# Kernel optimization log

Hardware: AMD Instinct MI355X
Metric: run time of the kernel (lower is better)

Reference implementation:

```python
import jax, jax.numpy as jnp
import numpy as np

N, E, G = 20000, 320000, 50
IN, H1, D1, H2, D2 = 64, 10, 64, 1, 128
NEG_SLOPE = 0.2  # DGL GATConv default


def _edge_softmax(e, dst, n):
    # segment softmax of per-edge scores e[E,H] grouped by destination node
    m = jax.ops.segment_max(e, dst, num_segments=n)
    m = jnp.where(jnp.isfinite(m), m, 0.0)  # nodes with zero in-degree
    ex = jnp.exp(e - m[dst])
    s = jax.ops.segment_sum(ex, dst, num_segments=n)
    return ex / jnp.where(s > 0, s, 1.0)[dst]


def _gat_layer(feat, W, al, ar, b, src, dst, n, h, d):
    ft = (feat @ W).reshape(n, h, d)              # [N,H,D]
    el = (ft * al).sum(-1)                        # [N,H]
    er = (ft * ar).sum(-1)                        # [N,H]
    e = jax.nn.leaky_relu(el[src] + er[dst], NEG_SLOPE)  # [E,H]
    a = _edge_softmax(e, dst, n)                  # [E,H]
    out = jax.ops.segment_sum(ft[src] * a[:, :, None], dst, num_segments=n)
    return out + b.reshape(1, h, d)


def setup_inputs() -> dict:
    key = jax.random.key(0)
    ks = jax.random.split(key, 16)
    feat = jax.random.normal(ks[0], (N, IN), dtype=jnp.float32)
    src = jax.random.randint(ks[1], (E,), 0, N)
    dst = jax.random.randint(ks[2], (E,), 0, N)
    graph_ids = jnp.sort(jax.random.randint(ks[3], (N,), 0, G))
    s1 = 1.0 / np.sqrt(IN)
    W1 = jax.random.normal(ks[4], (IN, H1 * D1), dtype=jnp.float32) * s1
    al1 = jax.random.normal(ks[5], (H1, D1), dtype=jnp.float32) * 0.1
    ar1 = jax.random.normal(ks[6], (H1, D1), dtype=jnp.float32) * 0.1
    b1 = jnp.zeros((H1 * D1,), dtype=jnp.float32)
    W2 = jax.random.normal(ks[7], (D1, H2 * D2), dtype=jnp.float32) * (1.0 / np.sqrt(D1))
    al2 = jax.random.normal(ks[8], (H2, D2), dtype=jnp.float32) * 0.1
    ar2 = jax.random.normal(ks[9], (H2, D2), dtype=jnp.float32) * 0.1
    b2 = jnp.zeros((H2 * D2,), dtype=jnp.float32)
    lw1 = jax.random.normal(ks[10], (D2, D2), dtype=jnp.float32) * (1.0 / np.sqrt(D2))
    lb1 = jnp.zeros((D2,), dtype=jnp.float32)
    lw2 = jax.random.normal(ks[11], (D2, 1), dtype=jnp.float32) * (1.0 / np.sqrt(D2))
    lb2 = jnp.zeros((1,), dtype=jnp.float32)
    return {"feat": feat, "src": src, "dst": dst, "graph_ids": graph_ids,
            "W1": W1, "al1": al1, "ar1": ar1, "b1": b1,
            "W2": W2, "al2": al2, "ar2": ar2, "b2": b2,
            "lw1": lw1, "lb1": lb1, "lw2": lw2, "lb2": lb2}


def reference(feat, src, dst, graph_ids, W1, al1, ar1, b1, W2, al2, ar2, b2, lw1, lb1, lw2, lb2):
    # eval mode: all dropouts are identity
    h = _gat_layer(feat, W1, al1, ar1, b1, src, dst, N, H1, D1)  # [N,10,64]
    h = jax.nn.relu(h)
    h = h.sum(axis=1)                                            # [N,64]
    h = _gat_layer(h, W2, al2, ar2, b2, src, dst, N, H2, D2)     # [N,1,128]
    h = jax.nn.relu(h)
    # readout_nodes op='max' over each graph in the batch
    r = jax.ops.segment_max(h, graph_ids, num_segments=G)        # [G,1,128]
    r = jnp.where(jnp.isfinite(r), r, 0.0)
    r = jax.nn.relu(r @ lw1 + lb1)
    r = jax.nn.relu(r @ lw2 + lb2)                               # [G,1,1]
    return r.reshape(-1)
```

## Files before the change

### kernel.cpp

```cpp
#include <hip/hip_runtime.h>
#include <hip/hip_fp16.h>

#define NN 20000
#define EE 320000
#define GG 50
#define IN_ 64
#define H1_ 10
#define D1_ 64
#define D2_ 128
#define F1 640
#define NEG 0.2f
#define CAP 128

static inline int cdiv(long long a, int b){ return (int)((a + b - 1) / b); }

__device__ inline float lrelu(float x){ return x > 0.f ? x : NEG * x; }

__device__ inline void fma_mix_lo(float& acc, float packed, float a){
  asm("v_fma_mix_f32 %0, %1, %2, %0 op_sel_hi:[1,0,0]"
      : "+v"(acc) : "v"(packed), "v"(a));
}
__device__ inline void fma_mix_hi(float& acc, float packed, float a){
  asm("v_fma_mix_f32 %0, %1, %2, %0 op_sel:[1,0,0] op_sel_hi:[1,0,0]"
      : "+v"(acc) : "v"(packed), "v"(a));
}

__global__ __launch_bounds__(256) void fused1(
    const int* __restrict__ src, const int* __restrict__ dst,
    int* __restrict__ cur, int* __restrict__ ssrc,
    const float* __restrict__ feat, const float* __restrict__ W1,
    const float* __restrict__ al1, const float* __restrict__ ar1,
    __half* __restrict__ ft1h, float* __restrict__ elT, float* __restrict__ erT){
  __shared__ float AsT[64][68];
  __shared__ __half Bsh[64][68];
  int b = blockIdx.x;
  if(b < 1250){
    int e = b * 256 + threadIdx.x;
    int d = dst[e];
    int pos = atomicAdd(&cur[d], 1);
    if(pos < CAP) ssrc[(d << 7) + pos] = src[e];
    return;
  }
  int b2 = b - 1250;
  int h = b2 % H1_;
  int n0 = (b2 / H1_) * 64;
  int tid = threadIdx.x;
  #pragma unroll
  for(int l = 0; l < 4; l++){
    int idx = tid + l * 256;
    int r = idx >> 4, c4 = (idx & 15) << 2;
    float4 v = make_float4(0.f,0.f,0.f,0.f);
    if(n0 + r < NN) v = *(const float4*)&feat[(size_t)(n0 + r) * IN_ + c4];
    AsT[c4+0][r] = v.x; AsT[c4+1][r] = v.y; AsT[c4+2][r] = v.z; AsT[c4+3][r] = v.w;
    float4 w = *(const float4*)&W1[(size_t)(idx >> 4) * F1 + h * 64 + c4];
    union { __half2 h2[2]; float2 f2; } u;
    u.h2[0] = __floats2half2_rn(w.x, w.y);
    u.h2[1] = __floats2half2_rn(w.z, w.w);
    *(float2*)&Bsh[idx >> 4][c4] = u.f2;
  }
  __syncthreads();
  int tr = tid >> 4, tc = tid & 15;
  float acc[4][4];
  #pragma unroll
  for(int i = 0; i < 4; i++)
    #pragma unroll
    for(int j = 0; j < 4; j++) acc[i][j] = 0.f;
  #pragma unroll 8
  for(int k = 0; k < 64; k++){
    float4 a4 = *(const float4*)&AsT[k][tr << 2];
    float2 b2v = *(const float2*)&Bsh[k][tc << 2];
    float av[4] = {a4.x, a4.y, a4.z, a4.w};
    #pragma unroll
    for(int i = 0; i < 4; i++){
      fma_mix_lo(acc[i][0], b2v.x, av[i]);
      fma_mix_hi(acc[i][1], b2v.x, av[i]);
      fma_mix_lo(acc[i][2], b2v.y, av[i]);
      fma_mix_hi(acc[i][3], b2v.y, av[i]);
    }
  }
  float al4[4], ar4[4];
  #pragma unroll
  for(int j = 0; j < 4; j++){
    al4[j] = al1[h * 64 + (tc << 2) + j];
    ar4[j] = ar1[h * 64 + (tc << 2) + j];
  }
  #pragma unroll
  for(int i = 0; i < 4; i++){
    int row = n0 + (tr << 2) + i;
    bool ok = row < NN;
    if(ok){
      union { __half2 h2[2]; float2 f2; } u;
      u.h2[0] = __floats2half2_rn(acc[i][0], acc[i][1]);
      u.h2[1] = __floats2half2_rn(acc[i][2], acc[i][3]);
      *(float2*)&ft1h[((size_t)h * NN + row) * 64 + (tc << 2)] = u.f2;
    }
    float e1 = acc[i][0]*al4[0] + acc[i][1]*al4[1] + acc[i][2]*al4[2] + acc[i][3]*al4[3];
    float e2 = acc[i][0]*ar4[0] + acc[i][1]*ar4[1] + acc[i][2]*ar4[2] + acc[i][3]*ar4[3];
    #pragma unroll
    for(int off = 1; off < 16; off <<= 1){
      e1 += __shfl_xor(e1, off, 64);
      e2 += __shfl_xor(e2, off, 64);
    }
    if(tc == 0 && ok){
      elT[(size_t)h * NN + row] = e1;
      erT[(size_t)h * NN + row] = e2;
    }
  }
}

__global__ __launch_bounds__(256) void l1_head(
    const int* __restrict__ cur, const int* __restrict__ ssrc,
    const float* __restrict__ elT, const float* __restrict__ erT,
    const __half* __restrict__ ft1h, const float* __restrict__ b1,
    __half* __restrict__ out1h){
  __shared__ int2 pairs[4][2][2][32];
  int b = blockIdx.x;
  int xcd = b & 7, slot = b >> 3;
  int h, blk;
  if(slot < 1250){ h = xcd; blk = slot; }
  else {
    int s = slot - 1250; h = 8 + (xcd >> 2); blk = (xcd & 3) * 313 + s;
    if(blk >= 1250) return;
  }
  int wave = threadIdx.x >> 6, lane = threadIdx.x & 63;
  int half = lane >> 5, l32 = lane & 31;
  int eg = l32 >> 4, dg = l32 & 15;
  int dnA = blk * 16 + wave * 4 + half * 2;
  int dnB = dnA + 1;
  int degA = min(cur[dnA], CAP), degB = min(cur[dnB], CAP);
  int baseA = dnA << 7, baseB = dnB << 7;
  float4 accA = make_float4(0.f,0.f,0.f,0.f);
  float4 accB = make_float4(0.f,0.f,0.f,0.f);
  const char* fbase = (const char*)(ft1h + (size_t)h * NN * 64) + (dg << 3);
  const float* elh = elT + (size_t)h * NN;
  float erA = erT[(size_t)h * NN + dnA];
  float erB = erT[(size_t)h * NN + dnB];
  int2* wpA = pairs[wave][half][0];
  int2* wpB = pairs[wave][half][1];

  if(__any(degA > 32 || degB > 32)){
    #pragma unroll
    for(int which = 0; which < 2; which++){
      int base = which ? baseB : baseA;
      int deg  = which ? degB : degA;
      float er_h = which ? erB : erA;
      float4* accp = which ? &accB : &accA;
      int2* wp = which ? wpB : wpA;
      float sm = 0.f;
      for(int i = l32; i < deg; i += 32)
        sm += __expf(lrelu(elh[ssrc[base + i]] + er_h));
      #pragma unroll
      for(int o = 1; o < 32; o <<= 1) sm += __shfl_xor(sm, o, 64);
      float inv = deg > 0 ? 1.f / sm : 0.f;
      for(int c = 0; c < deg; c += 32){
        int m = deg - c; if(m > 32) m = 32;
        if(l32 < m){
          int sn = ssrc[base + c + l32];
          wp[l32] = make_int2(__float_as_int(__expf(lrelu(elh[sn] + er_h)) * inv), sn << 7);
        }
        for(int i = eg; i < m; i += 2){
          int2 pr = wp[i];
          float a_i = __int_as_float(pr.x);
          float2 raw = *(const float2*)(fbase + pr.y);
          fma_mix_lo(accp->x, raw.x, a_i); fma_mix_hi(accp->y, raw.x, a_i);
          fma_mix_lo(accp->z, raw.y, a_i); fma_mix_hi(accp->w, raw.y, a_i);
        }
      }
    }
  } else {
    int snA = 0, snB = 0;
    if(l32 < degA) snA = ssrc[baseA + l32];
    if(l32 < degB) snB = ssrc[baseB + l32];
    float pA = 0.f, pB = 0.f;
    if(l32 < degA) pA = __expf(lrelu(elh[snA] + erA));
    if(l32 < degB) pB = __expf(lrelu(elh[snB] + erB));
    float smA = pA, smB = pB;
    #pragma unroll
    for(int o = 1; o < 32; o <<= 1){
      smA += __shfl_xor(smA, o, 64);
      smB += __shfl_xor(smB, o, 64);
    }
    float invA = degA > 0 ? 1.f / smA : 0.f;
    float invB = degB > 0 ? 1.f / smB : 0.f;
    wpA[l32] = l32 < degA ? make_int2(__float_as_int(pA * invA), snA << 7)
                          : make_int2(0, 0);
    wpB[l32] = l32 < degB ? make_int2(__float_as_int(pB * invB), snB << 7)
                          : make_int2(0, 0);
    int maxd = max(degA, degB);
    int i = eg;
    for(; i + 2 < maxd; i += 4){
      int2 a0 = wpA[i], a1 = wpA[i + 2];
      int2 b0 = wpB[i], b1 = wpB[i + 2];
      float2 ra0 = *(const float2*)(fbase + a0.y);
      float2 rb0 = *(const float2*)(fbase + b0.y);
      float2 ra1 = *(const float2*)(fbase + a1.y);
      float2 rb1 = *(const float2*)(fbase + b1.y);
      float aa0 = __int_as_float(a0.x), aa1 = __int_as_float(a1.x);
      float ab0 = __int_as_float(b0.x), ab1 = __int_as_float(b1.x);
      fma_mix_lo(accA.x, ra0.x, aa0); fma_mix_hi(accA.y, ra0.x, aa0);
      fma_mix_lo(accA.z, ra0.y, aa0); fma_mix_hi(accA.w, ra0.y, aa0);
      fma_mix_lo(accB.x, rb0.x, ab0); fma_mix_hi(accB.y, rb0.x, ab0);
      fma_mix_lo(accB.z, rb0.y, ab0); fma_mix_hi(accB.w, rb0.y, ab0);
      fma_mix_lo(accA.x, ra1.x, aa1); fma_mix_hi(accA.y, ra1.x, aa1);
      fma_mix_lo(accA.z, ra1.y, aa1); fma_mix_hi(accA.w, ra1.y, aa1);
      fma_mix_lo(accB.x, rb1.x, ab1); fma_mix_hi(accB.y, rb1.x, ab1);
      fma_mix_lo(accB.z, rb1.y, ab1); fma_mix_hi(accB.w, rb1.y, ab1);
    }
    if(i < maxd){
      int2 a0 = wpA[i], b0 = wpB[i];
      float2 ra0 = *(const float2*)(fbase + a0.y);
      float2 rb0 = *(const float2*)(fbase + b0.y);
      float aa0 = __int_as_float(a0.x), ab0 = __int_as_float(b0.x);
      fma_mix_lo(accA.x, ra0.x, aa0); fma_mix_hi(accA.y, ra0.x, aa0);
      fma_mix_lo(accA.z, ra0.y, aa0); fma_mix_hi(accA.w, ra0.y, aa0);
      fma_mix_lo(accB.x, rb0.x, ab0); fma_mix_hi(accB.y, rb0.x, ab0);
      fma_mix_lo(accB.z, rb0.y, ab0); fma_mix_hi(accB.w, rb0.y, ab0);
    }
  }
  accA.x += __shfl_xor(accA.x, 16, 64); accB.x += __shfl_xor(accB.x, 16, 64);
  accA.y += __shfl_xor(accA.y, 16, 64); accB.y += __shfl_xor(accB.y, 16, 64);
  accA.z += __shfl_xor(accA.z, 16, 64); accB.z += __shfl_xor(accB.z, 16, 64);
  accA.w += __shfl_xor(accA.w, 16, 64); accB.w += __shfl_xor(accB.w, 16, 64);
  if(eg == 0){
    int d = dg << 2;
    const float* bp = &b1[h * 64 + d];
    float b0 = bp[0], b1v = bp[1], b2v = bp[2], b3 = bp[3];
    union { __half2 h2[2]; float2 f2; } u;
    u.h2[0] = __floats2half2_rn(fmaxf(accA.x + b0, 0.f), fmaxf(accA.y + b1v, 0.f));
    u.h2[1] = __floats2half2_rn(fmaxf(accA.z + b2v, 0.f), fmaxf(accA.w + b3, 0.f));
    *(float2*)&out1h[(size_t)dnA * F1 + h * 64 + d] = u.f2;
    u.h2[0] = __floats2half2_rn(fmaxf(accB.x + b0, 0.f), fmaxf(accB.y + b1v, 0.f));
    u.h2[1] = __floats2half2_rn(fmaxf(accB.z + b2v, 0.f), fmaxf(accB.w + b3, 0.f));
    *(float2*)&out1h[(size_t)dnB * F1 + h * 64 + d] = u.f2;
  }
}

__global__ __launch_bounds__(256) void gemm2(
    const __half* __restrict__ out1h, const float* __restrict__ W2,
    const float* __restrict__ al2, const float* __restrict__ ar2,
    __half* __restrict__ ft2h, float* __restrict__ el, float* __restrict__ er){
  __shared__ float AsT[64][36];
  __shared__ __half Bsh[64][132];
  int n0 = blockIdx.x * 32;
  int tid = threadIdx.x;
  #pragma unroll
  for(int l = 0; l < 2; l++){
    int idx = tid + l * 256;
    int r = idx >> 4, c4 = (idx & 15) << 2;
    float4 sv = make_float4(0.f,0.f,0.f,0.f);
    if(n0 + r < NN){
      const __half* rp = &out1h[(size_t)(n0 + r) * F1 + c4];
      #pragma unroll
      for(int hh = 0; hh < H1_; hh++){
        float2 raw = *(const float2*)(rp + hh * 64);
        const __half2* hp = (const __half2*)&raw;
        float2 f0 = __half22float2(hp[0]);
        float2 f1 = __half22float2(hp[1]);
        sv.x += f0.x; sv.y += f0.y; sv.z += f1.x; sv.w += f1.y;
      }
    }
    AsT[c4+0][r] = sv.x; AsT[c4+1][r] = sv.y; AsT[c4+2][r] = sv.z; AsT[c4+3][r] = sv.w;
  }
  #pragma unroll
  for(int l = 0; l < 8; l++){
    int idx = tid + l * 256;
    int k = idx >> 5, c4 = (idx & 31) << 2;
    float4 w = *(const float4*)&W2[(size_t)k * D2_ + c4];
    union { __half2 h2[2]; float2 f2; } u;
    u.h2[0] = __floats2half2_rn(w.x, w.y);
    u.h2[1] = __floats2half2_rn(w.z, w.w);
    *(float2*)&Bsh[k][c4] = u.f2;
  }
  __syncthreads();
  int tr = tid >> 5, tc = tid & 31;
  float acc[4][4];
  #pragma unroll
  for(int i = 0; i < 4; i++)
    #pragma unroll
    for(int j = 0; j < 4; j++) acc[i][j] = 0.f;
  #pragma unroll 8
  for(int k = 0; k < 64; k++){
    float4 a4 = *(const float4*)&AsT[k][tr << 2];
    float2 b2v = *(const float2*)&Bsh[k][tc << 2];
    float av[4] = {a4.x, a4.y, a4.z, a4.w};
    #pragma unroll
    for(int i = 0; i < 4; i++){
      fma_mix_lo(acc[i][0], b2v.x, av[i]);
      fma_mix_hi(acc[i][1], b2v.x, av[i]);
      fma_mix_lo(acc[i][2], b2v.y, av[i]);
      fma_mix_hi(acc[i][3], b2v.y, av[i]);
    }
  }
  float al4[4], ar4[4];
  #pragma unroll
  for(int j = 0; j < 4; j++){
    al4[j] = al2[(tc << 2) + j];
    ar4[j] = ar2[(tc << 2) + j];
  }
  int col = tc << 2;
  int half = col >> 6, c64 = col & 63;
  #pragma unroll
  for(int i = 0; i < 4; i++){
    int row = n0 + (tr << 2) + i;
    bool ok = row < NN;
    if(ok){
      union { __half2 h2[2]; float2 f2; } u;
      u.h2[0] = __floats2half2_rn(acc[i][0], acc[i][1]);
      u.h2[1] = __floats2half2_rn(acc[i][2], acc[i][3]);
      *(float2*)&ft2h[((size_t)half * NN + row) * 64 + c64] = u.f2;
    }
    float e1 = acc[i][0]*al4[0] + acc[i][1]*al4[1] + acc[i][2]*al4[2] + acc[i][3]*al4[3];
    float e2 = acc[i][0]*ar4[0] + acc[i][1]*ar4[1] + acc[i][2]*ar4[2] + acc[i][3]*ar4[3];
    #pragma unroll
    for(int off = 1; off < 32; off <<= 1){
      e1 += __shfl_xor(e1, off, 64);
      e2 += __shfl_xor(e2, off, 64);
    }
    if(tc == 0 && ok){ el[row] = e1; er[row] = e2; }
  }
}

__global__ __launch_bounds__(256) void l2_head(
    const int* __restrict__ cur, const int* __restrict__ ssrc,
    const float* __restrict__ el, const float* __restrict__ er,
    const __half* __restrict__ ft2h, const float* __restrict__ b2,
    float* __restrict__ h2v){
  __shared__ int2 pairs[4][2][2][32];
  int b = blockIdx.x;
  int xcd = b & 7, slot = b >> 3;
  int halfd = xcd >> 2;
  int blk = (xcd & 3) * 313 + slot;
  if(blk >= 1250) return;
  int wave = threadIdx.x >> 6, lane = threadIdx.x & 63;
  int half = lane >> 5, l32 = lane & 31;
  int eg = l32 >> 4, dg = l32 & 15;
  int dnA = blk * 16 + wave * 4 + half * 2;
  int dnB = dnA + 1;
  int degA = min(cur[dnA], CAP), degB = min(cur[dnB], CAP);
  int baseA = dnA << 7, baseB = dnB << 7;
  float4 accA = make_float4(0.f,0.f,0.f,0.f);
  float4 accB = make_float4(0.f,0.f,0.f,0.f);
  const char* fbase = (const char*)(ft2h + (size_t)halfd * NN * 64) + (dg << 3);
  float erA = er[dnA], erB = er[dnB];
  int2* wpA = pairs[wave][half][0];
  int2* wpB = pairs[wave][half][1];

  if(__any(degA > 32 || degB > 32)){
    #pragma unroll
    for(int which = 0; which < 2; which++){
      int base = which ? baseB : baseA;
      int deg  = which ? degB : degA;
      float er_d = which ? erB : erA;
      float4* accp = which ? &accB : &accA;
      int2* wp = which ? wpB : wpA;
      float sm = 0.f;
      for(int i = l32; i < deg; i += 32)
        sm += __expf(lrelu(el[ssrc[base + i]] + er_d));
      #pragma unroll
      for(int o = 1; o < 32; o <<= 1) sm += __shfl_xor(sm, o, 64);
      float inv = deg > 0 ? 1.f / sm : 0.f;
      for(int c = 0; c < deg; c += 32){
        int m = deg - c; if(m > 32) m = 32;
        if(l32 < m){
          int sn = ssrc[base + c + l32];
          wp[l32] = make_int2(__float_as_int(__expf(lrelu(el[sn] + er_d)) * inv), sn << 7);
        }
        for(int i = eg; i < m; i += 2){
          int2 pr = wp[i];
          float a_i = __int_as_float(pr.x);
          float2 raw = *(const float2*)(fbase + pr.y);
          fma_mix_lo(accp->x, raw.x, a_i); fma_mix_hi(accp->y, raw.x, a_i);
          fma_mix_lo(accp->z, raw.y, a_i); fma_mix_hi(accp->w, raw.y, a_i);
        }
      }
    }
  } else {
    int snA = 0, snB = 0;
    if(l32 < degA) snA = ssrc[baseA + l32];
    if(l32 < degB) snB = ssrc[baseB + l32];
    float pA = 0.f, pB = 0.f;
    if(l32 < degA) pA = __expf(lrelu(el[snA] + erA));
    if(l32 < degB) pB = __expf(lrelu(el[snB] + erB));
    float smA = pA, smB = pB;
    #pragma unroll
    for(int o = 1; o < 32; o <<= 1){
      smA += __shfl_xor(smA, o, 64);
      smB += __shfl_xor(smB, o, 64);
    }
    float invA = degA > 0 ? 1.f / smA : 0.f;
    float invB = degB > 0 ? 1.f / smB : 0.f;
    wpA[l32] = l32 < degA ? make_int2(__float_as_int(pA * invA), snA << 7)
                          : make_int2(0, 0);
    wpB[l32] = l32 < degB ? make_int2(__float_as_int(pB * invB), snB << 7)
                          : make_int2(0, 0);
    int maxd = max(degA, degB);
    int i = eg;
    for(; i + 2 < maxd; i += 4){
      int2 a0 = wpA[i], a1 = wpA[i + 2];
      int2 b0 = wpB[i], b1 = wpB[i + 2];
      float2 ra0 = *(const float2*)(fbase + a0.y);
      float2 rb0 = *(const float2*)(fbase + b0.y);
      float2 ra1 = *(const float2*)(fbase + a1.y);
      float2 rb1 = *(const float2*)(fbase + b1.y);
      float aa0 = __int_as_float(a0.x), aa1 = __int_as_float(a1.x);
      float ab0 = __int_as_float(b0.x), ab1 = __int_as_float(b1.x);
      fma_mix_lo(accA.x, ra0.x, aa0); fma_mix_hi(accA.y, ra0.x, aa0);
      fma_mix_lo(accA.z, ra0.y, aa0); fma_mix_hi(accA.w, ra0.y, aa0);
      fma_mix_lo(accB.x, rb0.x, ab0); fma_mix_hi(accB.y, rb0.x, ab0);
      fma_mix_lo(accB.z, rb0.y, ab0); fma_mix_hi(accB.w, rb0.y, ab0);
      fma_mix_lo(accA.x, ra1.x, aa1); fma_mix_hi(accA.y, ra1.x, aa1);
      fma_mix_lo(accA.z, ra1.y, aa1); fma_mix_hi(accA.w, ra1.y, aa1);
      fma_mix_lo(accB.x, rb1.x, ab1); fma_mix_hi(accB.y, rb1.x, ab1);
      fma_mix_lo(accB.z, rb1.y, ab1); fma_mix_hi(accB.w, rb1.y, ab1);
    }
    if(i < maxd){
      int2 a0 = wpA[i], b0 = wpB[i];
      float2 ra0 = *(const float2*)(fbase + a0.y);
      float2 rb0 = *(const float2*)(fbase + b0.y);
      float aa0 = __int_as_float(a0.x), ab0 = __int_as_float(b0.x);
      fma_mix_lo(accA.x, ra0.x, aa0); fma_mix_hi(accA.y, ra0.x, aa0);
      fma_mix_lo(accA.z, ra0.y, aa0); fma_mix_hi(accA.w, ra0.y, aa0);
      fma_mix_lo(accB.x, rb0.x, ab0); fma_mix_hi(accB.y, rb0.x, ab0);
      fma_mix_lo(accB.z, rb0.y, ab0); fma_mix_hi(accB.w, rb0.y, ab0);
    }
  }
  accA.x += __shfl_xor(accA.x, 16, 64); accB.x += __shfl_xor(accB.x, 16, 64);
  accA.y += __shfl_xor(accA.y, 16, 64); accB.y += __shfl_xor(accB.y, 16, 64);
  accA.z += __shfl_xor(accA.z, 16, 64); accB.z += __shfl_xor(accB.z, 16, 64);
  accA.w += __shfl_xor(accA.w, 16, 64); accB.w += __shfl_xor(accB.w, 16, 64);
  if(eg == 0){
    int doff = halfd * 64 + (dg << 2);
    const float* bp = &b2[doff];
    float b0 = bp[0], b1v = bp[1], b2v = bp[2], b3 = bp[3];
    float4 o;
    o.x = fmaxf(accA.x + b0, 0.f);
    o.y = fmaxf(accA.y + b1v, 0.f);
    o.z = fmaxf(accA.z + b2v, 0.f);
    o.w = fmaxf(accA.w + b3, 0.f);
    *(float4*)&h2v[(size_t)dnA * D2_ + doff] = o;
    o.x = fmaxf(accB.x + b0, 0.f);
    o.y = fmaxf(accB.y + b1v, 0.f);
    o.z = fmaxf(accB.z + b2v, 0.f);
    o.w = fmaxf(accB.w + b3, 0.f);
    *(float4*)&h2v[(size_t)dnB * D2_ + doff] = o;
  }
}

__global__ __launch_bounds__(256) void readout(
    const float* __restrict__ h2v, const int* __restrict__ gid,
    const float* __restrict__ lw1, const float* __restrict__ lb1,
    const float* __restrict__ lw2, const float* __restrict__ lb2,
    float* __restrict__ out){
  __shared__ int sb[2];
  __shared__ float mx2[2][D2_];
  __shared__ float rv[D2_];
  __shared__ float t[D2_];
  int g = blockIdx.x, tid = threadIdx.x;
  int d = tid & 127, hh = tid >> 7;
  if(tid < 2){
    int tgt = g + tid;
    int lo = 0, hi = NN;
    while(lo < hi){ int mid = (lo + hi) >> 1; if(gid[mid] < tgt) lo = mid + 1; else hi = mid; }
    sb[tid] = lo;
  }
  __syncthreads();
  int gs = sb[0], ge = sb[1];
  float m0 = 0.f, m1 = 0.f, m2 = 0.f, m3 = 0.f;
  int n = gs + hh;
  for(; n + 6 < ge; n += 8){
    m0 = fmaxf(m0, h2v[(size_t)(n + 0) * D2_ + d]);
    m1 = fmaxf(m1, h2v[(size_t)(n + 2) * D2_ + d]);
    m2 = fmaxf(m2, h2v[(size_t)(n + 4) * D2_ + d]);
    m3 = fmaxf(m3, h2v[(size_t)(n + 6) * D2_ + d]);
  }
  for(; n < ge; n += 2) m0 = fmaxf(m0, h2v[(size_t)n * D2_ + d]);
  mx2[hh][d] = fmaxf(fmaxf(m0, m1), fmaxf(m2, m3));
  __syncthreads();
  if(tid < D2_) rv[d] = fmaxf(mx2[0][d], mx2[1][d]);
  __syncthreads();
  if(tid < D2_){
    float acc = lb1[d];
    #pragma unroll 8
    for(int k = 0; k < D2_; k++) acc += rv[k] * lw1[k * D2_ + d];
    acc = acc > 0.f ? acc : 0.f;
    t[d] = acc * lw2[d];
  }
  __syncthreads();
  for(int off = 64; off > 0; off >>= 1){
    if(tid < off) t[tid] += t[tid + off];
    __syncthreads();
  }
  if(tid == 0){
    float v = t[0] + lb2[0];
    out[g] = v > 0.f ? v : 0.f;
  }
}

extern "C" void kernel_launch(void* const* d_in, const int* in_sizes, int n_in,
                              void* d_out, int out_size, void* d_ws, size_t ws_size,
                              hipStream_t stream) {
  const float* feat = (const float*)d_in[0];
  const int*   src  = (const int*)d_in[1];
  const int*   dst  = (const int*)d_in[2];
  const int*   gid  = (const int*)d_in[3];
  const float* W1   = (const float*)d_in[4];
  const float* al1  = (const float*)d_in[5];
  const float* ar1  = (const float*)d_in[6];
  const float* b1   = (const float*)d_in[7];
  const float* W2   = (const float*)d_in[8];
  const float* al2  = (const float*)d_in[9];
  const float* ar2  = (const float*)d_in[10];
  const float* b2   = (const float*)d_in[11];
  const float* lw1  = (const float*)d_in[12];
  const float* lb1  = (const float*)d_in[13];
  const float* lw2  = (const float*)d_in[14];
  const float* lb2  = (const float*)d_in[15];
  float* out = (float*)d_out;

  float* ws = (float*)d_ws;
  size_t o = 0;
  __half* ft1h = (__half*)(ws + o); o += (size_t)NN * F1 / 2;
  __half* out1h = (__half*)(ws + o); o += (size_t)NN * F1 / 2;
  __half* ft2h = (__half*)(ws + o); o += (size_t)NN * D2_ / 2;
  float* h2v  = ws + o; o += (size_t)NN * D2_;
  float* el1  = ws + o; o += (size_t)NN * H1_;
  float* er1  = ws + o; o += (size_t)NN * H1_;
  float* el2  = ws + o; o += NN;
  float* er2  = ws + o; o += NN;
  int* cur    = (int*)(ws + o); o += NN;
  int* ssrc   = (int*)(ws + o); o += (size_t)NN * CAP;

  hipMemsetAsync(cur, 0, (size_t)NN * 4, stream);
  fused1<<<1250 + H1_ * cdiv(NN, 64), 256, 0, stream>>>(
      src, dst, cur, ssrc, feat, W1, al1, ar1, ft1h, el1, er1);
  l1_head<<<8 * (1250 + 313), 256, 0, stream>>>(cur, ssrc, el1, er1, ft1h, b1, out1h);
  gemm2<<<cdiv(NN, 32), 256, 0, stream>>>(out1h, W2, al2, ar2, ft2h, el2, er2);
  l2_head<<<8 * 313, 256, 0, stream>>>(cur, ssrc, el2, er2, ft2h, b2, h2v);
  readout<<<GG, 256, 0, stream>>>(h2v, gid, lw1, lb1, lw2, lb2, out);
}
```

Measured before the change: 165.3 us.

## Use MFMA f16 for layer-1 projection with fp16 pre-converted inputs

Adds a prep kernel that converts feat to fp16, transposes W1 to fp16, and zeroes the degree counters, replacing the memset. The fused1 GEMM moves from fma_mix VALU with LDS staging to 16x16x32 f16 MFMA, loading operands straight from global memory. Output is staged through LDS for coalesced fp16 stores. Attention logits are reduced by shuffles. This adds one extra kernel launch and an fp16 rounding of feat, which the old path kept in fp32.

Result: faster. 149.0 us (-9.8%).

```diff
diff --git a/kernel.cpp b/kernel.cpp
--- a/kernel.cpp
+++ b/kernel.cpp
@@ -14,6 +14,9 @@
 
 static inline int cdiv(long long a, int b){ return (int)((a + b - 1) / b); }
 
+typedef _Float16 half8 __attribute__((ext_vector_type(8)));
+typedef float f32x4 __attribute__((ext_vector_type(4)));
+
 __device__ inline float lrelu(float x){ return x > 0.f ? x : NEG * x; }
 
 __device__ inline void fma_mix_lo(float& acc, float packed, float a){
@@ -25,14 +28,34 @@
       : "+v"(acc) : "v"(packed), "v"(a));
 }
 
+__global__ __launch_bounds__(256) void prep(
+    const float* __restrict__ feat, const float* __restrict__ W1,
+    _Float16* __restrict__ featH, _Float16* __restrict__ W1T,
+    int* __restrict__ cur){
+  int b = blockIdx.x, t = threadIdx.x;
+  if(b < 1250){
+    int idx = b * 1024 + t * 4;
+    float4 v = *(const float4*)&feat[idx];
+    _Float16 h4[4] = {(_Float16)v.x, (_Float16)v.y, (_Float16)v.z, (_Float16)v.w};
+    *(float2*)&featH[idx] = *(float2*)h4;
+    if(t < 16) cur[b * 16 + t] = 0;
+  } else {
+    int idx = (b - 1250) * 1024 + t * 4;
+    int c = idx >> 6, k0 = idx & 63;
+    _Float16 h4[4];
+    #pragma unroll
+    for(int j = 0; j < 4; j++) h4[j] = (_Float16)W1[(size_t)(k0 + j) * F1 + c];
+    *(float2*)&W1T[idx] = *(float2*)h4;
+  }
+}
+
 __global__ __launch_bounds__(256) void fused1(
     const int* __restrict__ src, const int* __restrict__ dst,
     int* __restrict__ cur, int* __restrict__ ssrc,
-    const float* __restrict__ feat, const float* __restrict__ W1,
+    const _Float16* __restrict__ featH, const _Float16* __restrict__ W1T,
     const float* __restrict__ al1, const float* __restrict__ ar1,
-    __half* __restrict__ ft1h, float* __restrict__ elT, float* __restrict__ erT){
-  __shared__ float AsT[64][68];
-  __shared__ __half Bsh[64][68];
+    _Float16* __restrict__ ft1h, float* __restrict__ elT, float* __restrict__ erT){
+  __shared__ _Float16 sC[4][16][72];
   int b = blockIdx.x;
   if(b < 1250){
     int e = b * 256 + threadIdx.x;
@@ -44,67 +67,69 @@
   int b2 = b - 1250;
   int h = b2 % H1_;
   int n0 = (b2 / H1_) * 64;
-  int tid = threadIdx.x;
-  #pragma unroll
-  for(int l = 0; l < 4; l++){
-    int idx = tid + l * 256;
-    int r = idx >> 4, c4 = (idx & 15) << 2;
-    float4 v = make_float4(0.f,0.f,0.f,0.f);
-    if(n0 + r < NN) v = *(const float4*)&feat[(size_t)(n0 + r) * IN_ + c4];
-    AsT[c4+0][r] = v.x; AsT[c4+1][r] = v.y; AsT[c4+2][r] = v.z; AsT[c4+3][r] = v.w;
-    float4 w = *(const float4*)&W1[(size_t)(idx >> 4) * F1 + h * 64 + c4];
-    union { __half2 h2[2]; float2 f2; } u;
-    u.h2[0] = __floats2half2_rn(w.x, w.y);
-    u.h2[1] = __floats2half2_rn(w.z, w.w);
-    *(float2*)&Bsh[idx >> 4][c4] = u.f2;
-  }
+  int tid = threadIdx.x, w = tid >> 6, l = tid & 63;
+  int lr = l & 15, lk = l >> 4;
+  int r0 = n0 + w * 16;
+  int row = r0 + lr;
+  half8 a0 = {}, a1 = {};
+  if(row < NN){
+    a0 = *(const half8*)&featH[row * 64 + lk * 8];
+    a1 = *(const half8*)&featH[row * 64 + 32 + lk * 8];
+  }
+  f32x4 acc[4];
+  #pragma unroll
+  for(int c0 = 0; c0 < 4; c0++) acc[c0] = (f32x4){0.f, 0.f, 0.f, 0.f};
+  #pragma unroll
+  for(int c0 = 0; c0 < 4; c0++){
+    int col = h * 64 + c0 * 16 + lr;
+    half8 b0 = *(const half8*)&W1T[col * 64 + lk * 8];
+    half8 b1 = *(const half8*)&W1T[col * 64 + 32 + lk * 8];
+    acc[c0] = __builtin_amdgcn_mfma_f32_16x16x32_f16(a0, b0, acc[c0], 0, 0, 0);
+    acc[c0] = __builtin_amdgcn_mfma_f32_16x16x32_f16(a1, b1, acc[c0], 0, 0, 0);
+  }
+  float elp[4] = {0.f,0.f,0.f,0.f}, erp[4] = {0.f,0.f,0.f,0.f};
+  #pragma unroll
+  for(int c0 = 0; c0 < 4; c0++){
+    float al = al1[h * 64 + c0 * 16 + lr];
+    float ar = ar1[h * 64 + c0 * 16 + lr];
+    #pragma unroll
+    for(int j = 0; j < 4; j++){
+      elp[j] += acc[c0][j] * al;
+      erp[j] += acc[c0][j] * ar;
+    }
+  }
+  #pragma unroll
+  for(int off = 1; off < 16; off <<= 1){
+    #pragma unroll
+    for(int j = 0; j < 4; j++){
+      elp[j] += __shfl_xor(elp[j], off, 64);
+      erp[j] += __shfl_xor(erp[j], off, 64);
+    }
+  }
+  if(lr == 0){
+    #pragma unroll
+    for(int j = 0; j < 4; j++){
+      int rj = r0 + lk * 4 + j;
+      if(rj < NN){
+        elT[(size_t)h * NN + rj] = elp[j];
+        erT[(size_t)h * NN + rj] = erp[j];
+      }
+    }
+  }
+  #pragma unroll
+  for(int c0 = 0; c0 < 4; c0++)
+    #pragma unroll
+    for(int j = 0; j < 4; j++)
+      sC[w][lk * 4 + j][c0 * 16 + lr] = (_Float16)acc[c0][j];
   __syncthreads();
-  int tr = tid >> 4, tc = tid & 15;
-  float acc[4][4];
-  #pragma unroll
-  for(int i = 0; i < 4; i++)
-    #pragma unroll
-    for(int j = 0; j < 4; j++) acc[i][j] = 0.f;
-  #pragma unroll 8
-  for(int k = 0; k < 64; k++){
-    float4 a4 = *(const float4*)&AsT[k][tr << 2];
-    float2 b2v = *(const float2*)&Bsh[k][tc << 2];
-    float av[4] = {a4.x, a4.y, a4.z, a4.w};
-    #pragma unroll
-    for(int i = 0; i < 4; i++){
-      fma_mix_lo(acc[i][0], b2v.x, av[i]);
-      fma_mix_hi(acc[i][1], b2v.x, av[i]);
-      fma_mix_lo(acc[i][2], b2v.y, av[i]);
-      fma_mix_hi(acc[i][3], b2v.y, av[i]);
-    }
-  }
-  float al4[4], ar4[4];
-  #pragma unroll
-  for(int j = 0; j < 4; j++){
-    al4[j] = al1[h * 64 + (tc << 2) + j];
-    ar4[j] = ar1[h * 64 + (tc << 2) + j];
-  }
-  #pragma unroll
-  for(int i = 0; i < 4; i++){
-    int row = n0 + (tr << 2) + i;
-    bool ok = row < NN;
-    if(ok){
-      union { __half2 h2[2]; float2 f2; } u;
-      u.h2[0] = __floats2half2_rn(acc[i][0], acc[i][1]);
-      u.h2[1] = __floats2half2_rn(acc[i][2], acc[i][3]);
-      *(float2*)&ft1h[((size_t)h * NN + row) * 64 + (tc << 2)] = u.f2;
-    }
-    float e1 = acc[i][0]*al4[0] + acc[i][1]*al4[1] + acc[i][2]*al4[2] + acc[i][3]*al4[3];
-    float e2 = acc[i][0]*ar4[0] + acc[i][1]*ar4[1] + acc[i][2]*ar4[2] + acc[i][3]*ar4[3];
-    #pragma unroll
-    for(int off = 1; off < 16; off <<= 1){
-      e1 += __shfl_xor(e1, off, 64);
-      e2 += __shfl_xor(e2, off, 64);
-    }
-    if(tc == 0 && ok){
-      elT[(size_t)h * NN + row] = e1;
-      erT[(size_t)h * NN + row] = e2;
-    }
+  #pragma unroll
+  for(int it = 0; it < 2; it++){
+    int idx = l + it * 64;
+    int orow = idx >> 3, oc = (idx & 7) * 8;
+    int grow = r0 + orow;
+    if(grow < NN)
+      *(float4*)&ft1h[((size_t)h * NN + grow) * 64 + oc] =
+          *(const float4*)&sC[w][orow][oc];
   }
 }
 
@@ -519,7 +544,7 @@
 
   float* ws = (float*)d_ws;
   size_t o = 0;
-  __half* ft1h = (__half*)(ws + o); o += (size_t)NN * F1 / 2;
+  _Float16* ft1h = (_Float16*)(ws + o); o += (size_t)NN * F1 / 2;
   __half* out1h = (__half*)(ws + o); o += (size_t)NN * F1 / 2;
   __half* ft2h = (__half*)(ws + o); o += (size_t)NN * D2_ / 2;
   float* h2v  = ws + o; o += (size_t)NN * D2_;
@@ -529,11 +554,14 @@
   float* er2  = ws + o; o += NN;
   int* cur    = (int*)(ws + o); o += NN;
   int* ssrc   = (int*)(ws + o); o += (size_t)NN * CAP;
-
-  hipMemsetAsync(cur, 0, (size_t)NN * 4, stream);
+  _Float16* featH = (_Float16*)(ws + o); o += (size_t)NN * IN_ / 2;
+  _Float16* W1T   = (_Float16*)(ws + o); o += (size_t)F1 * IN_ / 2;
+
+  prep<<<1290, 256, 0, stream>>>(feat, W1, featH, W1T, cur);
   fused1<<<1250 + H1_ * cdiv(NN, 64), 256, 0, stream>>>(
-      src, dst, cur, ssrc, feat, W1, al1, ar1, ft1h, el1, er1);
-  l1_head<<<8 * (1250 + 313), 256, 0, stream>>>(cur, ssrc, el1, er1, ft1h, b1, out1h);
+      src, dst, cur, ssrc, featH, W1T, al1, ar1, ft1h, el1, er1);
+  l1_head<<<8 * (1250 + 313), 256, 0, stream>>>(cur, ssrc, el1, er1,
+                                                (const __half*)ft1h, b1, out1h);
   gemm2<<<cdiv(NN, 32), 256, 0, stream>>>(out1h, W2, al2, ar2, ft2h, el2, er2);
   l2_head<<<8 * 313, 256, 0, stream>>>(cur, ssrc, el2, er2, ft2h, b2, h2v);
   readout<<<GG, 256, 0, stream>>>(h2v, gid, lw1, lb1, lw2, lb2, out);
```
